# Optimization experiments

Measured on AMD Instinct MI355X. Metric: run time of the kernel, lower is better.

## Reference

```python
import jax, jax.numpy as jnp
from jax import lax
import numpy as np

# Geometry fixed by __init__ (see shape_source)
UP = 2          # up_factor[0]
DOWN = 2        # down_factor[0]
PAD_LO = 11
PAD_HI = 10
SLOPE = 0.2
GAIN = np.sqrt(2.0).astype(np.float32)


def _kaiser_beta(atten):
    if atten > 50:
        return 0.1102 * (atten - 8.7)
    if atten > 21:
        return 0.5842 * (atten - 21.0) ** 0.4 + 0.07886 * (atten - 21.0)
    return 0.0


def _firwin(numtaps, cutoff, width, fs):
    # numpy re-implementation of scipy.signal.firwin(numtaps, cutoff, width=width, fs=fs)
    nyq = fs / 2.0
    atten = 2.285 * (numtaps - 1) * np.pi * (width / nyq) + 7.95  # kaiser_atten
    beta = _kaiser_beta(atten)
    m = np.arange(numtaps) - (numtaps - 1) / 2.0
    fc = cutoff / nyq
    h = fc * np.sinc(fc * m) * np.kaiser(numtaps, beta)
    h = h / h.sum()  # unity DC gain (pass_zero scaling)
    return h.astype(np.float32)


def _depthwise_conv1d(x, f, axis, stride=1, lhs_dilation=1, padding=(0, 0)):
    """Depthwise 1D FIR along spatial `axis` (2 or 3) of NCHW tensor.
    Filter is flipped (true convolution, as in upfirdn2d)."""
    C = x.shape[1]
    k = f.shape[0]
    fr = f[::-1]
    if axis == 2:
        kern = jnp.broadcast_to(fr.reshape(1, 1, k, 1), (C, 1, k, 1))
        strides, ld, pads = (stride, 1), (lhs_dilation, 1), [padding, (0, 0)]
    else:
        kern = jnp.broadcast_to(fr.reshape(1, 1, 1, k), (C, 1, 1, k))
        strides, ld, pads = (1, stride), (1, lhs_dilation), [(0, 0), padding]
    return lax.conv_general_dilated(
        x, kern, window_strides=strides, padding=pads, lhs_dilation=ld,
        dimension_numbers=('NCHW', 'OIHW', 'NCHW'), feature_group_count=C)


def setup_inputs() -> dict:
    key = jax.random.key(0)
    k1, k2 = jax.random.split(key)
    x = jax.random.normal(k1, (32, 128, 64, 64), dtype=jnp.float32)
    bias = jax.random.normal(k2, (128,), dtype=jnp.float32) * 0.1
    # up filter: numtaps=12, cutoff=in_cutoff=28, width=2*in_half_width=8, fs=tmp_sr=128
    up_filter = jnp.asarray(_firwin(12, 28.0, 8.0, 128.0))
    # down filter: numtaps=12, cutoff=out_cutoff=28, width=2*out_half_width=8, fs=128
    down_filter = jnp.asarray(_firwin(12, 28.0, 8.0, 128.0))
    return {"x": x, "bias": bias, "up_filter": up_filter, "down_filter": down_filter}


def reference(x, bias, up_filter, down_filter):
    # filtered_lrelu reference: upfirdn2d(up, fu, gain=up**2) -> bias -> lrelu*sqrt(2) -> upfirdn2d(down, fd)
    # Zero-insertion upsampling fused via lhs_dilation; dilated length is H*UP-(UP-1),
    # so the trailing UP-1 zeros of the nominal H*UP upsampled signal move into pad_hi.
    fu = up_filter * UP  # gain up per separable pass -> up**2 total
    pad = (PAD_LO, PAD_HI + UP - 1)
    y = _depthwise_conv1d(x, fu, axis=2, lhs_dilation=UP, padding=pad)
    y = _depthwise_conv1d(y, fu, axis=3, lhs_dilation=UP, padding=pad)  # [B,C,138,138]
    y = y + bias[None, :, None, None]
    y = jnp.where(y >= 0, y, SLOPE * y) * GAIN
    y = _depthwise_conv1d(y, down_filter, axis=2, stride=DOWN)
    y = _depthwise_conv1d(y, down_filter, axis=3, stride=DOWN)  # [B,C,64,64]
    return y
```

## Files before the change

### kernel.cpp

```cpp
#include <hip/hip_runtime.h>


#define NT 512
#define GAIN 1.41421356237309504880f
#define C1 (0.6f * GAIN)
#define C2 (0.4f * GAIN)

#define ZROWS 42
#define ZSTRIDE 84
#define ZPAD 8
#define YSTRIDE 148
#define YWSTRIDE 68

#define ZB_OFF 0
#define YB_OFF (ZROWS * ZSTRIDE)
#define YW_OFF 0
#define LDS_FLOATS (YB_OFF + ZROWS * YSTRIDE)

__device__ __forceinline__ float sload(float v) {
    return __uint_as_float(__builtin_amdgcn_readfirstlane(__float_as_uint(v)));
}

__global__ __launch_bounds__(NT, 8) void fused_upfirdn_lrelu(
    const float* __restrict__ x,
    const float* __restrict__ bias,
    const float* __restrict__ upf,
    const float* __restrict__ dnf,
    float* __restrict__ out)
{
    extern __shared__ float lds[];
    float* zb = lds + ZB_OFF;
    float* yb = lds + YB_OFF;
    float* yw = lds + YW_OFF;

    const int t = threadIdx.x;
    const int bid = blockIdx.x;
    const int s = bid >> 2;
    const int o0 = (bid & 3) << 4;
    const int c = s & 127;

    float fu[12], fd[12];
#pragma unroll
    for (int j = 0; j < 12; ++j) {
        fu[j] = sload(2.0f * upf[j]);
        fd[j] = sload(dnf[j]);
    }
    const float bv = sload(bias[c]);

    const float* xg = x + (size_t)s * 4096;
    float* outg = out + (size_t)s * 4096;

    if (t < 336) {
        const int m = t >> 4;
        const int c4 = (t & 15) << 2;
        const int M = o0 + m;
        float4 xv[6];
        if (M >= 5 && M <= 63) {
#pragma unroll
            for (int d = 0; d < 6; ++d)
                xv[d] = *reinterpret_cast<const float4*>(xg + (M - 5 + d) * 64 + c4);
        } else {
#pragma unroll
            for (int d = 0; d < 6; ++d) {
                const int r = M - 5 + d;
                xv[d] = (r >= 0 && r <= 63)
                      ? *reinterpret_cast<const float4*>(xg + r * 64 + c4)
                      : make_float4(0.f, 0.f, 0.f, 0.f);
            }
        }
        float a0[4] = {0,0,0,0}, a1[4] = {0,0,0,0};
#pragma unroll
        for (int d = 0; d < 6; ++d) {
            const float w0 = fu[2 * (5 - d)], w1 = fu[2 * (5 - d) + 1];
            a0[0] += w0 * xv[d].x; a0[1] += w0 * xv[d].y; a0[2] += w0 * xv[d].z; a0[3] += w0 * xv[d].w;
            a1[0] += w1 * xv[d].x; a1[1] += w1 * xv[d].y; a1[2] += w1 * xv[d].z; a1[3] += w1 * xv[d].w;
        }
        float* zr = zb + (2 * m) * ZSTRIDE + ZPAD + c4;
        *reinterpret_cast<float4*>(zr)           = make_float4(a0[0], a0[1], a0[2], a0[3]);
        *reinterpret_cast<float4*>(zr + ZSTRIDE) = make_float4(a1[0], a1[1], a1[2], a1[3]);
    } else {
        for (int pt = t - 336; pt < 210; pt += 176) {
            const int rl = pt / 5;
            const int p = pt - rl * 5;
            const int col = (p < 2) ? (p << 2) : (72 + ((p - 2) << 2));
            *reinterpret_cast<float4*>(zb + rl * ZSTRIDE + col) = make_float4(0.f, 0.f, 0.f, 0.f);
        }
    }
    __syncthreads();

    if (t < 378) {
        const int cg = t / 42;
        const int il = t - cg * 42;
        const int mbase = cg << 3;
        const float* zr = zb + il * ZSTRIDE + mbase;
        float zv[16];
#pragma unroll
        for (int q = 0; q < 4; ++q) {
            const float4 v = *reinterpret_cast<const float4*>(zr + (q << 2));
            zv[4 * q] = v.x; zv[4 * q + 1] = v.y; zv[4 * q + 2] = v.z; zv[4 * q + 3] = v.w;
        }
        float yv[16];
#pragma unroll
        for (int e = 0; e < 8; ++e) {
            float a0 = bv, a1 = bv;
#pragma unroll
            for (int tt = 0; tt < 6; ++tt) {
                const float zz = zv[8 + e - tt];
                a0 += fu[2 * tt]     * zz;
                a1 += fu[2 * tt + 1] * zz;
            }
            yv[2 * e]     = C1 * a0 + C2 * fabsf(a0);
            yv[2 * e + 1] = C1 * a1 + C2 * fabsf(a1);
        }
        float* yr = yb + il * YSTRIDE + (mbase << 1);
#pragma unroll
        for (int q = 0; q < 4; ++q)
            *reinterpret_cast<float4*>(yr + (q << 2)) =
                make_float4(yv[4 * q], yv[4 * q + 1], yv[4 * q + 2], yv[4 * q + 3]);
    }
    __syncthreads();

    if (t < 336) {
        const int cg = t / 42;
        const int il = t - cg * 42;
        const float* yr = yb + il * YSTRIDE + (cg << 4);
        float w[28];
#pragma unroll
        for (int q = 0; q < 7; ++q) {
            const float4 v = *reinterpret_cast<const float4*>(yr + (q << 2));
            w[4 * q] = v.x; w[4 * q + 1] = v.y; w[4 * q + 2] = v.z; w[4 * q + 3] = v.w;
        }
        float rv[8];
#pragma unroll
        for (int e = 0; e < 8; ++e) {
            float a = 0.0f;
#pragma unroll
            for (int j = 0; j < 12; ++j) a += fd[j] * w[2 * e + 11 - j];
            rv[e] = a;
        }
        float* wr = yw + il * YWSTRIDE + (cg << 3);
        *reinterpret_cast<float4*>(wr)     = make_float4(rv[0], rv[1], rv[2], rv[3]);
        *reinterpret_cast<float4*>(wr + 4) = make_float4(rv[4], rv[5], rv[6], rv[7]);
    }
    __syncthreads();

    if (t < 256) {
        const int o = t >> 4;
        const int col4 = (t & 15) << 2;
        const float* wr = yw + (2 * o) * YWSTRIDE + col4;
        float a0 = 0.f, a1 = 0.f, a2 = 0.f, a3 = 0.f;
#pragma unroll
        for (int rr = 0; rr < 12; ++rr) {
            const float4 v = *reinterpret_cast<const float4*>(wr + rr * YWSTRIDE);
            const float ww = fd[11 - rr];
            a0 += ww * v.x; a1 += ww * v.y; a2 += ww * v.z; a3 += ww * v.w;
        }
        *reinterpret_cast<float4*>(outg + (o0 + o) * 64 + col4) =
            make_float4(a0, a1, a2, a3);
    }
}

extern "C" void kernel_launch(void* const* d_in, const int* in_sizes, int n_in,
                              void* d_out, int out_size, void* d_ws, size_t ws_size,
                              hipStream_t stream) {
    const float* x    = (const float*)d_in[0];
    const float* bias = (const float*)d_in[1];
    const float* upf  = (const float*)d_in[2];
    const float* dnf  = (const float*)d_in[3];
    float* out = (float*)d_out;

    const int n_blocks = 32 * 128 * 4;
    const size_t lds_bytes = (size_t)LDS_FLOATS * sizeof(float);
    hipLaunchKernelGGL(fused_upfirdn_lrelu, dim3(n_blocks), dim3(NT),
                       lds_bytes, stream, x, bias, upf, dnf, out);
}
```

Baseline: 73.24 us.

## Assign row bands per wavefront to drop intermediate block barriers

Remaps the three horizontal stages so each of seven wavefronts owns a fixed band of six intermediate rows. Each wave then produces and consumes only its own LDS data, so two of the three __syncthreads are removed and the block shrinks to 448 threads. The vertical downsampling stage now reuses the z buffer region and has 128 threads each compute two output rows, sharing loaded rows between them. The risk is correctness: it depends on wave-local ordering of LDS reads and writes without explicit barriers, and lanes go unused inside each wave.

```diff
diff --git a/kernel.cpp b/kernel.cpp
--- a/kernel.cpp
+++ b/kernel.cpp
@@ -1,7 +1,7 @@
 #include <hip/hip_runtime.h>
 
 
-#define NT 512
+#define NT 448
 #define GAIN 1.41421356237309504880f
 #define C1 (0.6f * GAIN)
 #define C2 (0.4f * GAIN)
@@ -10,18 +10,17 @@
 #define ZSTRIDE 84
 #define ZPAD 8
 #define YSTRIDE 148
-#define YWSTRIDE 68
+#define YWSTRIDE 84
 
 #define ZB_OFF 0
 #define YB_OFF (ZROWS * ZSTRIDE)
-#define YW_OFF 0
 #define LDS_FLOATS (YB_OFF + ZROWS * YSTRIDE)
 
 __device__ __forceinline__ float sload(float v) {
     return __uint_as_float(__builtin_amdgcn_readfirstlane(__float_as_uint(v)));
 }
 
-__global__ __launch_bounds__(NT, 8) void fused_upfirdn_lrelu(
+__global__ __launch_bounds__(NT, 7) void fused_upfirdn_lrelu(
     const float* __restrict__ x,
     const float* __restrict__ bias,
     const float* __restrict__ upf,
@@ -31,9 +30,10 @@
     extern __shared__ float lds[];
     float* zb = lds + ZB_OFF;
     float* yb = lds + YB_OFF;
-    float* yw = lds + YW_OFF;
 
     const int t = threadIdx.x;
+    const int w = t >> 6;
+    const int l = t & 63;
     const int bid = blockIdx.x;
     const int s = bid >> 2;
     const int o0 = (bid & 3) << 4;
@@ -50,9 +50,10 @@
     const float* xg = x + (size_t)s * 4096;
     float* outg = out + (size_t)s * 4096;
 
-    if (t < 336) {
-        const int m = t >> 4;
-        const int c4 = (t & 15) << 2;
+    if (l < 48) {
+        const int ml = l >> 4;
+        const int c4 = (l & 15) << 2;
+        const int m = 3 * w + ml;
         const int M = o0 + m;
         float4 xv[6];
         if (M >= 5 && M <= 63) {
@@ -79,18 +80,18 @@
         *reinterpret_cast<float4*>(zr)           = make_float4(a0[0], a0[1], a0[2], a0[3]);
         *reinterpret_cast<float4*>(zr + ZSTRIDE) = make_float4(a1[0], a1[1], a1[2], a1[3]);
     } else {
-        for (int pt = t - 336; pt < 210; pt += 176) {
-            const int rl = pt / 5;
-            const int p = pt - rl * 5;
-            const int col = (p < 2) ? (p << 2) : (72 + ((p - 2) << 2));
-            *reinterpret_cast<float4*>(zb + rl * ZSTRIDE + col) = make_float4(0.f, 0.f, 0.f, 0.f);
+        for (int pi = l - 48; pi < 24; pi += 16) {
+            const int rl = pi >> 2;
+            const int pp = pi & 3;
+            const int col = (pp < 2) ? (pp << 2) : (64 + ((pp - 2) << 2) + 8);
+            *reinterpret_cast<float4*>(zb + (6 * w + rl) * ZSTRIDE + col) =
+                make_float4(0.f, 0.f, 0.f, 0.f);
         }
     }
-    __syncthreads();
 
-    if (t < 378) {
-        const int cg = t / 42;
-        const int il = t - cg * 42;
+    if (l < 54) {
+        const int cg = l / 6;
+        const int il = 6 * w + (l - cg * 6);
         const int mbase = cg << 3;
         const float* zr = zb + il * ZSTRIDE + mbase;
         float zv[16];
@@ -118,45 +119,52 @@
             *reinterpret_cast<float4*>(yr + (q << 2)) =
                 make_float4(yv[4 * q], yv[4 * q + 1], yv[4 * q + 2], yv[4 * q + 3]);
     }
-    __syncthreads();
 
-    if (t < 336) {
-        const int cg = t / 42;
-        const int il = t - cg * 42;
+    if (l < 48) {
+        const int cg = l / 6;
+        const int il = 6 * w + (l - cg * 6);
         const float* yr = yb + il * YSTRIDE + (cg << 4);
-        float w[28];
+        float wv[28];
 #pragma unroll
         for (int q = 0; q < 7; ++q) {
             const float4 v = *reinterpret_cast<const float4*>(yr + (q << 2));
-            w[4 * q] = v.x; w[4 * q + 1] = v.y; w[4 * q + 2] = v.z; w[4 * q + 3] = v.w;
+            wv[4 * q] = v.x; wv[4 * q + 1] = v.y; wv[4 * q + 2] = v.z; wv[4 * q + 3] = v.w;
         }
         float rv[8];
 #pragma unroll
         for (int e = 0; e < 8; ++e) {
             float a = 0.0f;
 #pragma unroll
-            for (int j = 0; j < 12; ++j) a += fd[j] * w[2 * e + 11 - j];
+            for (int j = 0; j < 12; ++j) a += fd[j] * wv[2 * e + 11 - j];
             rv[e] = a;
         }
-        float* wr = yw + il * YWSTRIDE + (cg << 3);
+        float* wr = zb + il * YWSTRIDE + (cg << 3);
         *reinterpret_cast<float4*>(wr)     = make_float4(rv[0], rv[1], rv[2], rv[3]);
         *reinterpret_cast<float4*>(wr + 4) = make_float4(rv[4], rv[5], rv[6], rv[7]);
     }
+
     __syncthreads();
 
-    if (t < 256) {
-        const int o = t >> 4;
+    if (t < 128) {
+        const int eg = t >> 4;
         const int col4 = (t & 15) << 2;
-        const float* wr = yw + (2 * o) * YWSTRIDE + col4;
-        float a0 = 0.f, a1 = 0.f, a2 = 0.f, a3 = 0.f;
+        const float* wr = zb + (eg << 2) * YWSTRIDE + col4;
+        float aA[4] = {0,0,0,0}, aB[4] = {0,0,0,0};
 #pragma unroll
-        for (int rr = 0; rr < 12; ++rr) {
-            const float4 v = *reinterpret_cast<const float4*>(wr + rr * YWSTRIDE);
-            const float ww = fd[11 - rr];
-            a0 += ww * v.x; a1 += ww * v.y; a2 += ww * v.z; a3 += ww * v.w;
+        for (int r = 0; r < 14; ++r) {
+            const float4 v = *reinterpret_cast<const float4*>(wr + r * YWSTRIDE);
+            if (r < 12) {
+                const float ww = fd[11 - r];
+                aA[0] += ww * v.x; aA[1] += ww * v.y; aA[2] += ww * v.z; aA[3] += ww * v.w;
+            }
+            if (r >= 2) {
+                const float ww = fd[13 - r];
+                aB[0] += ww * v.x; aB[1] += ww * v.y; aB[2] += ww * v.z; aB[3] += ww * v.w;
+            }
         }
-        *reinterpret_cast<float4*>(outg + (o0 + o) * 64 + col4) =
-            make_float4(a0, a1, a2, a3);
+        float* orow = outg + (o0 + (eg << 1)) * 64 + col4;
+        *reinterpret_cast<float4*>(orow)      = make_float4(aA[0], aA[1], aA[2], aA[3]);
+        *reinterpret_cast<float4*>(orow + 64) = make_float4(aB[0], aB[1], aB[2], aB[3]);
     }
 }
 
```

Result: slower. 77.77 us (+6.2%).
